# Kernel optimization log

Measured on AMD Instinct MI355X. Metric: run time of the kernel, lower is better.

Reference implementation:

```python
import jax, jax.numpy as jnp
import numpy as np

V, B, N, D, L, H = 30522, 32, 512, 512, 4, 8
HD = D // H
REC = L // 2  # block-recurrent layer index
SCALE = HD ** -0.5


def _ln(x, g, b):
    m = x.mean(-1, keepdims=True)
    v = ((x - m) ** 2).mean(-1, keepdims=True)
    return (x - m) / jnp.sqrt(v + 1e-5) * g + b


def _rope(t):
    # t: [b,h,n,hd]; rotary embedding on token positions (split-half convention)
    n = t.shape[2]
    inv = 1.0 / (10000.0 ** (jnp.arange(0, HD, 2, dtype=jnp.float32) / HD))
    f = jnp.arange(n, dtype=jnp.float32)[:, None] * inv  # [n, hd/2]
    cos, sin = jnp.cos(f), jnp.sin(f)
    t1, t2 = t[..., : HD // 2], t[..., HD // 2 :]
    return jnp.concatenate([t1 * cos - t2 * sin, t2 * cos + t1 * sin], -1)


def _heads(x):
    b, n, _ = x.shape
    return x.reshape(b, n, H, HD).transpose(0, 2, 1, 3)


def _merge(x):
    b, h, n, d = x.shape
    return x.transpose(0, 2, 1, 3).reshape(b, n, h * d)


def _attn(q, k, v, mask):
    s = jnp.einsum('bhid,bhjd->bhij', q, k) * SCALE
    if mask is not None:
        s = jnp.where(mask, s, jnp.float32(-1e9))
    a = jax.nn.softmax(s, axis=-1)
    return jnp.einsum('bhij,bhjd->bhid', a, v)


def setup_inputs() -> dict:
    key = jax.random.key(0)
    ks = jax.random.split(key, 12)
    w = lambda k, shp: jax.random.normal(k, shp, jnp.float32) * 0.02
    return {
        'ids': jax.random.randint(ks[0], (B, N), 0, V),
        'state': jax.random.normal(ks[1], (B, D), jnp.float32),
        'tok_emb': w(ks[2], (V, D)),
        'ln1_g': jnp.ones((L, D), jnp.float32), 'ln1_b': jnp.zeros((L, D), jnp.float32),
        'w_qkv': w(ks[3], (L, D, 3 * D)),
        'w_o': w(ks[4], (L, D, D)),
        'ln2_g': jnp.ones((L, D), jnp.float32), 'ln2_b': jnp.zeros((L, D), jnp.float32),
        'w_ff1': w(ks[5], (L, D, 4 * D)), 'b_ff1': jnp.zeros((L, 4 * D), jnp.float32),
        'w_ff2': w(ks[6], (L, 4 * D, D)), 'b_ff2': jnp.zeros((L, D), jnp.float32),
        's_ln_g': jnp.ones((D,), jnp.float32), 's_ln_b': jnp.zeros((D,), jnp.float32),
        'w_s_qkv': w(ks[7], (D, 3 * D)),
        'w_so': w(ks[8], (D, D)),
        'gate_beta': w(ks[9], (D,)),
        'f_ln_g': jnp.ones((D,), jnp.float32), 'f_ln_b': jnp.zeros((D,), jnp.float32),
        'head_w': w(ks[10], (D, 1)), 'head_b': jnp.zeros((1,), jnp.float32),
    }


def reference(ids, state, tok_emb, ln1_g, ln1_b, w_qkv, w_o, ln2_g, ln2_b,
              w_ff1, b_ff1, w_ff2, b_ff2, s_ln_g, s_ln_b, w_s_qkv, w_so,
              gate_beta, f_ln_g, f_ln_b, head_w, head_b):
    x = tok_emb[ids]                       # [b,n,d]
    s = state[:, None, :]                  # [b,1,d]  (state.unsqueeze(1))
    n = x.shape[1]
    causal = jnp.tril(jnp.ones((n, n), bool))
    for l in range(L):
        h = _ln(x, ln1_g[l], ln1_b[l])
        q, k, v = jnp.split(h @ w_qkv[l], 3, axis=-1)
        q, k, v = _heads(q), _heads(k), _heads(v)
        q, k = _rope(q), _rope(k)
        if l == REC:
            sn = _ln(s, s_ln_g, s_ln_b)
            sq, sk, sv = jnp.split(sn @ w_s_qkv, 3, axis=-1)
            sq, sk, sv = _heads(sq), _heads(sk), _heads(sv)
            # tokens attend over [tokens (causal), state vector (always visible)]
            m = jnp.concatenate([causal, jnp.ones((n, 1), bool)], axis=1)
            out_x = _attn(q, jnp.concatenate([k, sk], 2), jnp.concatenate([v, sv], 2), m)
            x = x + _merge(out_x) @ w_o[l]
            # state attends over [state, all tokens] (no mask)
            out_s = _attn(sq, jnp.concatenate([sk, k], 2), jnp.concatenate([sv, v], 2), None)
            upd = _merge(out_s) @ w_so
            g = jax.nn.sigmoid(gate_beta)   # fixed learned-EMA gate
            s = s * g + upd * (1.0 - g)
        else:
            out_x = _attn(q, k, v, causal)
            x = x + _merge(out_x) @ w_o[l]
        h2 = _ln(x, ln2_g[l], ln2_b[l])
        x = x + jax.nn.gelu(h2 @ w_ff1[l] + b_ff1[l]) @ w_ff2[l] + b_ff2[l]
    x = _ln(x, f_ln_g, f_ln_b)
    state_out = s[:, 0, :]                 # state[0].squeeze()
    logits = x @ head_w + head_b           # [b,n,1]
    out = jax.nn.log_softmax(logits, axis=-1)
    return out, state_out
```

## Files before the change

### kernel.cpp

```cpp
#include <hip/hip_runtime.h>
#include <hip/hip_bf16.h>
#include <math.h>

#define B_ 32
#define N_ 512
#define D_ 512
#define H_ 8
#define HD_ 64
#define QKV_ 1536
#define SCALE_ 0.125f

typedef unsigned short u16;
typedef unsigned int u32;
typedef __attribute__((ext_vector_type(8))) short bf16x8;
typedef __attribute__((ext_vector_type(4))) float f32x4;

#define GLOBAL_AS __attribute__((address_space(1)))
#define LDS_AS __attribute__((address_space(3)))

__device__ __forceinline__ float gelu_f(float x) {
  float u = 0.7978845608028654f * (x + 0.044715f * x * x * x);
  u = fminf(fmaxf(u, -15.f), 15.f);
  float e = __expf(2.f * u);
  float th = 1.f - 2.f * __builtin_amdgcn_rcpf(e + 1.f);
  return 0.5f * x * (1.0f + th);
}

__device__ __forceinline__ u16 f2b(float f) {
  union { float f; u32 u; } v;
  v.f = f;
  u32 r = (v.u + 0x7FFFu + ((v.u >> 16) & 1u)) >> 16;
  return (u16)r;
}

__device__ __forceinline__ float b2f(u16 x) {
  union { u32 u; float f; } v;
  v.u = ((u32)x) << 16;
  return v.f;
}

__device__ __forceinline__ int xcd_swz(int orig, int nwg) {
  int q = nwg >> 3, r = nwg & 7;
  int xcd = orig & 7, idx = orig >> 3;
  return (xcd < r ? xcd * (q + 1) : r * (q + 1) + (xcd - r) * q) + idx;
}

__global__ void k_prep(const float* __restrict__ w_qkv, const float* __restrict__ w_o,
                       const float* __restrict__ w_ff1, const float* __restrict__ w_ff2,
                       u16* __restrict__ wq_t, u16* __restrict__ wo_t,
                       u16* __restrict__ wf1_t, u16* __restrict__ wf2_t,
                       float* __restrict__ out0, float2* __restrict__ tab) {
  __shared__ float tile[32][33];
  int bid = blockIdx.x;
  int t = threadIdx.x;
  if (bid < 64) {
    int idx = bid * 256 + t;
    out0[idx] = 0.f;
    int n = idx >> 5, i = idx & 31;
    float inv = powf(10000.0f, -(float)i * (1.0f / 32.0f));
    float f = (float)n * inv;
    float s, c;
    sincosf(f, &s, &c);
    tab[idx] = make_float2(c, s);
    return;
  }
  int b2 = bid - 64;
  const float* W;
  u16* Wt;
  int K, N;
  if (b2 < 2304) {
    int l = b2 / 768; b2 -= l * 768;
    W = w_qkv + (size_t)l * D_ * QKV_; Wt = wq_t + (size_t)l * QKV_ * D_;
    K = D_; N = QKV_;
  } else if (b2 < 2816) {
    b2 -= 2304; int l = b2 >> 8; b2 &= 255;
    W = w_o + (size_t)l * D_ * D_; Wt = wo_t + (size_t)l * D_ * D_;
    K = D_; N = D_;
  } else if (b2 < 4864) {
    b2 -= 2816; int l = b2 >> 10; b2 &= 1023;
    W = w_ff1 + (size_t)l * D_ * 4 * D_; Wt = wf1_t + (size_t)l * 4 * D_ * D_;
    K = D_; N = 4 * D_;
  } else {
    b2 -= 4864; int l = b2 >> 10; b2 &= 1023;
    W = w_ff2 + (size_t)l * 4 * D_ * D_; Wt = wf2_t + (size_t)l * D_ * 4 * D_;
    K = 4 * D_; N = D_;
  }
  int nbx = N >> 5;
  int bx = b2 % nbx, by = b2 / nbx;
  int k0 = by * 32, n0 = bx * 32;
  int r = t >> 3, c4 = (t & 7) * 4;
  float4 v = *(const float4*)&W[(size_t)(k0 + r) * N + n0 + c4];
  tile[r][c4] = v.x; tile[r][c4 + 1] = v.y; tile[r][c4 + 2] = v.z; tile[r][c4 + 3] = v.w;
  __syncthreads();
  ushort4 o;
  o.x = f2b(tile[c4 + 0][r]); o.y = f2b(tile[c4 + 1][r]);
  o.z = f2b(tile[c4 + 2][r]); o.w = f2b(tile[c4 + 3][r]);
  *(ushort4*)&Wt[(size_t)(n0 + r) * K + k0 + c4] = o;
}

__global__ void k_embed(const int* __restrict__ ids, const float* __restrict__ emb,
                        float* __restrict__ x) {
  int row = blockIdx.x;
  int id = ids[row];
  const float4* s = (const float4*)(emb + (size_t)id * D_);
  float4* d = (float4*)(x + (size_t)row * D_);
  d[threadIdx.x] = s[threadIdx.x];
}

template <int BF16OUT>
__global__ void k_ln(const float* __restrict__ in, const float* __restrict__ gw,
                     const float* __restrict__ bw, void* __restrict__ outv) {
  int row = blockIdx.x * 4 + (threadIdx.x >> 6);
  int lane = threadIdx.x & 63;
  const float* p = in + (size_t)row * D_ + lane * 8;
  float4 v0 = *(const float4*)p;
  float4 v1 = *(const float4*)(p + 4);
  float s = v0.x + v0.y + v0.z + v0.w + v1.x + v1.y + v1.z + v1.w;
  float q = v0.x * v0.x + v0.y * v0.y + v0.z * v0.z + v0.w * v0.w +
            v1.x * v1.x + v1.y * v1.y + v1.z * v1.z + v1.w * v1.w;
#pragma unroll
  for (int o = 32; o >= 1; o >>= 1) {
    s += __shfl_xor(s, o);
    q += __shfl_xor(q, o);
  }
  float mean = s * (1.0f / D_);
  float var = q * (1.0f / D_) - mean * mean;
  float rstd = rsqrtf(var + 1e-5f);
  float4 g0 = *(const float4*)(gw + lane * 8);
  float4 g1 = *(const float4*)(gw + lane * 8 + 4);
  float4 b0 = *(const float4*)(bw + lane * 8);
  float4 b1 = *(const float4*)(bw + lane * 8 + 4);
  float o8[8];
  o8[0] = (v0.x - mean) * rstd * g0.x + b0.x;
  o8[1] = (v0.y - mean) * rstd * g0.y + b0.y;
  o8[2] = (v0.z - mean) * rstd * g0.z + b0.z;
  o8[3] = (v0.w - mean) * rstd * g0.w + b0.w;
  o8[4] = (v1.x - mean) * rstd * g1.x + b1.x;
  o8[5] = (v1.y - mean) * rstd * g1.y + b1.y;
  o8[6] = (v1.z - mean) * rstd * g1.z + b1.z;
  o8[7] = (v1.w - mean) * rstd * g1.w + b1.w;
  if (BF16OUT) {
    u16* op = (u16*)outv + (size_t)row * D_ + lane * 8;
    ushort4 a, b;
    a.x = f2b(o8[0]); a.y = f2b(o8[1]); a.z = f2b(o8[2]); a.w = f2b(o8[3]);
    b.x = f2b(o8[4]); b.y = f2b(o8[5]); b.z = f2b(o8[6]); b.w = f2b(o8[7]);
    *(ushort4*)op = a;
    *(ushort4*)(op + 4) = b;
  } else {
    float* op = (float*)outv + (size_t)row * D_ + lane * 8;
    *(float4*)op = make_float4(o8[0], o8[1], o8[2], o8[3]);
    *(float4*)(op + 4) = make_float4(o8[4], o8[5], o8[6], o8[7]);
  }
}

template <int EPI, int BF16OUT>
__global__ __launch_bounds__(256) void k_mgemm(
    const u16* __restrict__ A, const u16* __restrict__ Bt,
    const float* __restrict__ bias, const float* __restrict__ resid,
    void* __restrict__ Cv, int M, int K, int Nc, int nb0) {
  __shared__ u16 As[2][128 * 32];
  __shared__ u16 Bs[2][128 * 32];
  int t = threadIdx.x;
  int wave = t >> 6, lane = t & 63;
  int nwg = gridDim.x * gridDim.y;
  int swz = xcd_swz(blockIdx.y * gridDim.x + blockIdx.x, nwg);
  int m0 = (swz / gridDim.x) * 128;
  int n0 = ((swz % gridDim.x) + nb0) * 128;
  int wr = wave >> 1, wc = wave & 1;
  f32x4 acc[4][4] = {};

  int srow = lane >> 2;
  int scol = (lane & 3) * 8;
  const u16* gaBase = A + (size_t)(m0 + wave * 32 + srow) * K + scol;
  const u16* gbBase = Bt + (size_t)(n0 + wave * 32 + srow) * K + scol;

#define STAGE_MG(bsel, kk)                                                     \
  {                                                                            \
    _Pragma("unroll") for (int i_ = 0; i_ < 2; ++i_) {                         \
      int rbase_ = wave * 32 + i_ * 16;                                        \
      __builtin_amdgcn_global_load_lds(                                        \
          (const GLOBAL_AS void*)(gaBase + (size_t)(i_ * 16) * K + (kk)),      \
          (LDS_AS void*)&As[bsel][rbase_ * 32], 16, 0, 0);                     \
      __builtin_amdgcn_global_load_lds(                                        \
          (const GLOBAL_AS void*)(gbBase + (size_t)(i_ * 16) * K + (kk)),      \
          (LDS_AS void*)&Bs[bsel][rbase_ * 32], 16, 0, 0);                     \
    }                                                                          \
  }

  int nIter = K >> 5;
  STAGE_MG(0, 0);
  __syncthreads();
  for (int it = 0; it < nIter; ++it) {
    int cur = it & 1;
    if (it + 1 < nIter) STAGE_MG(cur ^ 1, (it + 1) << 5);
    const u16* as = As[cur];
    const u16* bs = Bs[cur];
    bf16x8 af[4], bfr[4];
#pragma unroll
    for (int mi = 0; mi < 4; ++mi)
      af[mi] = *(const bf16x8*)&as[(wr * 64 + mi * 16 + (lane & 15)) * 32 + (lane >> 4) * 8];
#pragma unroll
    for (int ni = 0; ni < 4; ++ni)
      bfr[ni] = *(const bf16x8*)&bs[(wc * 64 + ni * 16 + (lane & 15)) * 32 + (lane >> 4) * 8];
#pragma unroll
    for (int mi = 0; mi < 4; ++mi)
#pragma unroll
      for (int ni = 0; ni < 4; ++ni)
        acc[mi][ni] = __builtin_amdgcn_mfma_f32_16x16x32_bf16(bfr[ni], af[mi], acc[mi][ni], 0, 0, 0);
    __syncthreads();
  }
#undef STAGE_MG

#pragma unroll
  for (int mi = 0; mi < 4; ++mi) {
    int m = m0 + wr * 64 + mi * 16 + (lane & 15);
    size_t rowoff = (size_t)m * Nc;
#pragma unroll
    for (int ni = 0; ni < 4; ++ni) {
      int n = n0 + wc * 64 + ni * 16 + (lane >> 4) * 4;
      float v0 = acc[mi][ni][0], v1 = acc[mi][ni][1],
            v2 = acc[mi][ni][2], v3 = acc[mi][ni][3];
      if (EPI == 2 || EPI == 3) {
        float4 bb = *(const float4*)&bias[n];
        v0 += bb.x; v1 += bb.y; v2 += bb.z; v3 += bb.w;
      }
      if (EPI == 2) {
        v0 = gelu_f(v0); v1 = gelu_f(v1); v2 = gelu_f(v2); v3 = gelu_f(v3);
      }
      if (EPI == 1 || EPI == 3) {
        float4 rr = *(const float4*)&resid[rowoff + n];
        v0 += rr.x; v1 += rr.y; v2 += rr.z; v3 += rr.w;
      }
      if (BF16OUT) {
        ushort4 o;
        o.x = f2b(v0); o.y = f2b(v1); o.z = f2b(v2); o.w = f2b(v3);
        *(ushort4*)&((u16*)Cv)[rowoff + n] = o;
      } else {
        *(float4*)&((float*)Cv)[rowoff + n] = make_float4(v0, v1, v2, v3);
      }
    }
  }
}

template <int EPI>
__global__ __launch_bounds__(256) void k_gemm(const float* __restrict__ A,
                                              const float* __restrict__ W,
                                              const float* __restrict__ bias,
                                              const float* __restrict__ resid,
                                              float* __restrict__ C,
                                              int M, int K, int Nc) {
  __shared__ float As[32][68];
  __shared__ float Bs[32][68];
  int t = threadIdx.x;
  int tx = t & 15, ty = t >> 4;
  int m0 = blockIdx.y * 64, n0 = blockIdx.x * 64;
  float acc[4][4] = {};
  int ar = t >> 2, akc = (t & 3) * 8;
  int bkr = t >> 3, bnc = (t & 7) * 8;
  int garow = m0 + ar;
  bool aval = garow < M;
  const float* Aptr = A + (size_t)(aval ? garow : 0) * K + akc;
  const float* Wptr = W + (size_t)bkr * Nc + n0 + bnc;

  for (int k0 = 0; k0 < K; k0 += 32) {
    float4 a0, a1;
    if (aval) {
      a0 = *(const float4*)(Aptr + k0);
      a1 = *(const float4*)(Aptr + k0 + 4);
    } else {
      a0 = make_float4(0.f, 0.f, 0.f, 0.f);
      a1 = a0;
    }
    As[akc + 0][ar] = a0.x; As[akc + 1][ar] = a0.y;
    As[akc + 2][ar] = a0.z; As[akc + 3][ar] = a0.w;
    As[akc + 4][ar] = a1.x; As[akc + 5][ar] = a1.y;
    As[akc + 6][ar] = a1.z; As[akc + 7][ar] = a1.w;
    float4 b0 = *(const float4*)(Wptr + (size_t)k0 * Nc);
    float4 b1 = *(const float4*)(Wptr + (size_t)k0 * Nc + 4);
    *(float4*)&Bs[bkr][bnc] = b0;
    *(float4*)&Bs[bkr][bnc + 4] = b1;
    __syncthreads();
#pragma unroll
    for (int k = 0; k < 32; ++k) {
      float4 av = *(float4*)&As[k][ty * 4];
      float4 bv = *(float4*)&Bs[k][tx * 4];
      float a[4] = {av.x, av.y, av.z, av.w};
      float b[4] = {bv.x, bv.y, bv.z, bv.w};
#pragma unroll
      for (int i = 0; i < 4; ++i)
#pragma unroll
        for (int j = 0; j < 4; ++j) acc[i][j] += a[i] * b[j];
    }
    __syncthreads();
  }
#pragma unroll
  for (int i = 0; i < 4; ++i) {
    int m = m0 + ty * 4 + i;
    if (m >= M) break;
    size_t off = (size_t)m * Nc + n0 + tx * 4;
    float r[4];
#pragma unroll
    for (int j = 0; j < 4; ++j) {
      float v = acc[i][j];
      if (EPI == 2 || EPI == 3) v += bias[n0 + tx * 4 + j];
      if (EPI == 2) v = gelu_f(v);
      if (EPI == 1 || EPI == 3) v += resid[off + j];
      r[j] = v;
    }
    *(float4*)&C[off] = make_float4(r[0], r[1], r[2], r[3]);
  }
}

__global__ __launch_bounds__(512) void k_fattn(const u16* __restrict__ qkv,
                                               const float2* __restrict__ tab,
                                               u16* __restrict__ out) {
  __shared__ u16 Kl[64 * 64];
  __shared__ u16 Vt[64 * 64];
  __shared__ u16 Pl[8][16 * 64];
  int swz = xcd_swz(blockIdx.x, gridDim.x);
  int qt = swz & 3, h = (swz >> 2) & 7, b = swz >> 5;
  int t = threadIdx.x;
  int w = t >> 6, lane = t & 63;
  int c = lane & 15, g = lane >> 4;

  bf16x8 qa[2];
  {
    int n = qt * 128 + w * 16 + c;
    const u16* qptr = qkv + (size_t)(b * N_ + n) * QKV_ + h * HD_ + g * 8;
    union { bf16x8 v; u16 s[8]; } a0, a1, r0, r1;
    a0.v = *(const bf16x8*)qptr;
    a1.v = *(const bf16x8*)(qptr + 32);
    const float2* tb = tab + n * 32 + g * 8;
#pragma unroll
    for (int j = 0; j < 8; ++j) {
      float2 cs = tb[j];
      float lo = b2f(a0.s[j]), hi = b2f(a1.s[j]);
      r0.s[j] = f2b(lo * cs.x - hi * cs.y);
      r1.s[j] = f2b(hi * cs.x + lo * cs.y);
    }
    qa[0] = r0.v;
    qa[1] = r1.v;
  }

  f32x4 O[4] = {};
  float m_r[4], l_r[4];
#pragma unroll
  for (int r = 0; r < 4; ++r) { m_r[r] = -1e30f; l_r[r] = 0.f; }

  int myblk = 2 * qt + (w >> 2);
  int ktmax = 2 * qt + 1;

  for (int kt = 0; kt <= ktmax; ++kt) {
    if (t < 256) {
      int r = t >> 2, i0 = (t & 3) * 8;
      int n = kt * 64 + r;
      const u16* base = qkv + (size_t)(b * N_ + n) * QKV_ + D_ + h * HD_;
      union { bf16x8 v; u16 s[8]; } lo, hi, olo, ohi;
      lo.v = *(const bf16x8*)(base + i0);
      hi.v = *(const bf16x8*)(base + i0 + 32);
      const float2* tb = tab + n * 32 + i0;
#pragma unroll
      for (int j = 0; j < 8; ++j) {
        float2 cs = tb[j];
        float fl = b2f(lo.s[j]), fh = b2f(hi.s[j]);
        olo.s[j] = f2b(fl * cs.x - fh * cs.y);
        ohi.s[j] = f2b(fh * cs.x + fl * cs.y);
      }
      int bb = r * 128 + i0 * 2, sw = (r & 7) << 4;
      *(bf16x8*)((char*)Kl + (bb ^ sw)) = olo.v;
      *(bf16x8*)((char*)Kl + ((bb + 64) ^ sw)) = ohi.v;
    } else {
      int tt = t - 256;
      int kp = (tt >> 3) * 2, d0 = (tt & 7) * 8;
      const u16* v0p = qkv + (size_t)(b * N_ + kt * 64 + kp) * QKV_ + 2 * D_ + h * HD_ + d0;
      const u16* v1p = v0p + QKV_;
      ushort4 x0a = *(const ushort4*)v0p, x0b = *(const ushort4*)(v0p + 4);
      ushort4 x1a = *(const ushort4*)v1p, x1b = *(const ushort4*)(v1p + 4);
      u16 a0[8] = {x0a.x, x0a.y, x0a.z, x0a.w, x0b.x, x0b.y, x0b.z, x0b.w};
      u16 a1[8] = {x1a.x, x1a.y, x1a.z, x1a.w, x1b.x, x1b.y, x1b.z, x1b.w};
      u32* VtW = (u32*)Vt;
#pragma unroll
      for (int j = 0; j < 8; ++j) {
        int d = d0 + j;
        VtW[(d * 32 + (kp >> 1)) ^ ((d & 7) << 2)] = ((u32)a1[j] << 16) | (u32)a0[j];
      }
    }
    __syncthreads();

    if (kt <= myblk) {
      f32x4 s[4] = {};
#pragma unroll
      for (int ks = 0; ks < 2; ++ks) {
#pragma unroll
        for (int nt = 0; nt < 4; ++nt) {
          int krow = nt * 16 + c;
          int byteoff = (krow * 128 + (g * 8 + ks * 32) * 2) ^ ((krow & 7) << 4);
          bf16x8 kb = *(const bf16x8*)((const char*)Kl + byteoff);
          s[nt] = __builtin_amdgcn_mfma_f32_16x16x32_bf16(qa[ks], kb, s[nt], 0, 0, 0);
        }
      }
#pragma unroll
      for (int nt = 0; nt < 4; ++nt)
#pragma unroll
        for (int r = 0; r < 4; ++r) s[nt][r] *= SCALE_;
      if (kt == myblk) {
#pragma unroll
        for (int nt = 0; nt < 4; ++nt)
#pragma unroll
          for (int r = 0; r < 4; ++r)
            if (kt * 64 + nt * 16 + c > qt * 128 + w * 16 + g * 4 + r) s[nt][r] = -1e30f;
      }
      float tm[4], tl[4], fac[4];
#pragma unroll
      for (int r = 0; r < 4; ++r)
        tm[r] = fmaxf(fmaxf(s[0][r], s[1][r]), fmaxf(s[2][r], s[3][r]));
#pragma unroll
      for (int msk = 1; msk <= 8; msk <<= 1)
#pragma unroll
        for (int r = 0; r < 4; ++r)
          tm[r] = fmaxf(tm[r], __shfl_xor(tm[r], msk));
#pragma unroll
      for (int r = 0; r < 4; ++r) {
        float mn = fmaxf(m_r[r], tm[r]);
        fac[r] = __expf(m_r[r] - mn);
        m_r[r] = mn;
        tl[r] = 0.f;
      }
      u16* plw = Pl[w];
#pragma unroll
      for (int nt = 0; nt < 4; ++nt) {
#pragma unroll
        for (int r = 0; r < 4; ++r) {
          float p = __expf(s[nt][r] - m_r[r]);
          tl[r] += p;
          int q = g * 4 + r, kk = nt * 16 + c;
          plw[(q * 64 + kk) ^ ((q & 7) << 3)] = f2b(p);
        }
      }
#pragma unroll
      for (int msk = 1; msk <= 8; msk <<= 1)
#pragma unroll
        for (int r = 0; r < 4; ++r) tl[r] += __shfl_xor(tl[r], msk);
#pragma unroll
      for (int r = 0; r < 4; ++r) l_r[r] = l_r[r] * fac[r] + tl[r];
#pragma unroll
      for (int nt = 0; nt < 4; ++nt)
#pragma unroll
        for (int r = 0; r < 4; ++r) O[nt][r] *= fac[r];

#pragma unroll
      for (int ks = 0; ks < 2; ++ks) {
        int pbyte = (c * 128 + (g * 8 + ks * 32) * 2) ^ ((c & 7) << 4);
        bf16x8 pa = *(const bf16x8*)((const char*)plw + pbyte);
#pragma unroll
        for (int nt = 0; nt < 4; ++nt) {
          int d = nt * 16 + c;
          int vbyte = (d * 128 + (g * 8 + ks * 32) * 2) ^ ((d & 7) << 4);
          bf16x8 vb = *(const bf16x8*)((const char*)Vt + vbyte);
          O[nt] = __builtin_amdgcn_mfma_f32_16x16x32_bf16(pa, vb, O[nt], 0, 0, 0);
        }
      }
    }
    __syncthreads();
  }

  u16* dst = out + (size_t)(b * N_ + qt * 128 + w * 16) * D_ + h * HD_;
#pragma unroll
  for (int nt = 0; nt < 4; ++nt) {
#pragma unroll
    for (int r = 0; r < 4; ++r) {
      int q = g * 4 + r;
      dst[(size_t)q * D_ + nt * 16 + c] = f2b(O[nt][r] / l_r[r]);
    }
  }
}

__global__ __launch_bounds__(128) void k_state_attn(const float* __restrict__ sqkv,
                                                    const u16* __restrict__ qkv,
                                                    const float2* __restrict__ tab,
                                                    float* __restrict__ outs) {
  int h = blockIdx.x, b = blockIdx.y;
  __shared__ float sq[HD_];
  __shared__ float sc[513];
  __shared__ float red[128];
  int t = threadIdx.x;
  if (t < HD_) sq[t] = sqkv[(size_t)b * QKV_ + h * HD_ + t];
  __syncthreads();
  for (int j = t; j < 513; j += 128) {
    float acc = 0.f;
    if (j == 0) {
      const float* kp = sqkv + (size_t)b * QKV_ + D_ + h * HD_;
#pragma unroll
      for (int d = 0; d < HD_; ++d) acc += sq[d] * kp[d];
    } else {
      const u16* kp = qkv + (size_t)(b * N_ + j - 1) * QKV_ + D_ + h * HD_;
      const float2* tb = tab + (size_t)(j - 1) * 32;
#pragma unroll
      for (int d = 0; d < 32; ++d) {
        float2 cs = tb[d];
        float klo = b2f(kp[d]), khi = b2f(kp[d + 32]);
        acc += sq[d] * (klo * cs.x - khi * cs.y) + sq[d + 32] * (khi * cs.x + klo * cs.y);
      }
    }
    sc[j] = acc * SCALE_;
  }
  __syncthreads();
  float m = -1e30f;
  for (int j = t; j < 513; j += 128) m = fmaxf(m, sc[j]);
  red[t] = m;
  __syncthreads();
  for (int s = 64; s > 0; s >>= 1) {
    if (t < s) red[t] = fmaxf(red[t], red[t + s]);
    __syncthreads();
  }
  m = red[0];
  __syncthreads();
  float sum = 0.f;
  for (int j = t; j < 513; j += 128) {
    float p = expf(sc[j] - m);
    sc[j] = p;
    sum += p;
  }
  red[t] = sum;
  __syncthreads();
  for (int s = 64; s > 0; s >>= 1) {
    if (t < s) red[t] += red[t + s];
    __syncthreads();
  }
  float tot = red[0];
  if (t < HD_) {
    int d = t;
    float acc = sc[0] * sqkv[(size_t)b * QKV_ + 2 * D_ + h * HD_ + d];
    for (int j = 1; j <= N_; ++j)
      acc += sc[j] * b2f(qkv[(size_t)(b * N_ + j - 1) * QKV_ + 2 * D_ + h * HD_ + d]);
    outs[(size_t)b * D_ + h * HD_ + d] = acc / tot;
  }
}

__global__ void k_gate(const float* __restrict__ state, const float* __restrict__ upd,
                       const float* __restrict__ beta, float* __restrict__ out2) {
  int idx = blockIdx.x * 256 + threadIdx.x;
  int c = idx & (D_ - 1);
  float g = __builtin_amdgcn_rcpf(1.0f + __expf(-beta[c]));
  out2[idx] = state[idx] * g + upd[idx] * (1.0f - g);
}

extern "C" void kernel_launch(void* const* d_in, const int* in_sizes, int n_in,
                              void* d_out, int out_size, void* d_ws, size_t ws_size,
                              hipStream_t stream) {
  (void)in_sizes; (void)n_in; (void)out_size; (void)ws_size;
  const int* ids = (const int*)d_in[0];
  const float* state = (const float*)d_in[1];
  const float* tok_emb = (const float*)d_in[2];
  const float* ln1_g = (const float*)d_in[3];
  const float* ln1_b = (const float*)d_in[4];
  const float* w_qkv = (const float*)d_in[5];
  const float* w_o = (const float*)d_in[6];
  const float* ln2_g = (const float*)d_in[7];
  const float* ln2_b = (const float*)d_in[8];
  const float* w_ff1 = (const float*)d_in[9];
  const float* b_ff1 = (const float*)d_in[10];
  const float* w_ff2 = (const float*)d_in[11];
  const float* b_ff2 = (const float*)d_in[12];
  const float* s_ln_g = (const float*)d_in[13];
  const float* s_ln_b = (const float*)d_in[14];
  const float* w_s_qkv = (const float*)d_in[15];
  const float* w_so = (const float*)d_in[16];
  const float* gate_beta = (const float*)d_in[17];

  float* out0 = (float*)d_out;
  float* out1 = (float*)d_out + 16384;

  float* ws = (float*)d_ws;
  float* x = ws;
  u16* qkv_bf = (u16*)(ws + 8388608);
  u16* mid_bf = qkv_bf;
  u16* h_bf = (u16*)(ws + 25165824);
  u16* ao_bf = (u16*)(ws + 29360128);
  u16* wq_t = (u16*)(ws + 33554432);
  u16* wo_t = (u16*)(ws + 34734080);
  u16* wf1_t = (u16*)(ws + 34996224);
  u16* wf2_t = (u16*)(ws + 36044800);
  float* sln = ws + 37093376;
  float* sqkv = sln + 16384;
  float* souts = sqkv + 49152;
  float* supd = souts + 16384;
  float2* tab = (float2*)(ws + 37191680);

  const int M = B_ * N_;

  k_prep<<<dim3(6976), dim3(256), 0, stream>>>(w_qkv, w_o, w_ff1, w_ff2,
                                               wq_t, wo_t, wf1_t, wf2_t, out0, tab);
  k_embed<<<dim3(M), dim3(128), 0, stream>>>(ids, tok_emb, x);

  for (int l = 0; l < 3; ++l) {
    k_ln<1><<<dim3(M / 4), dim3(256), 0, stream>>>(x, ln1_g + l * D_, ln1_b + l * D_, h_bf);
    if (l == 2) {
      k_mgemm<0, 1><<<dim3(8, 128), dim3(256), 0, stream>>>(
          h_bf, wq_t + (size_t)l * QKV_ * D_, nullptr, nullptr, qkv_bf, M, D_, QKV_, 4);
      break;
    }
    k_mgemm<0, 1><<<dim3(12, 128), dim3(256), 0, stream>>>(
        h_bf, wq_t + (size_t)l * QKV_ * D_, nullptr, nullptr, qkv_bf, M, D_, QKV_, 0);
    k_fattn<<<dim3((N_ / 128) * H_ * B_), dim3(512), 0, stream>>>(qkv_bf, tab, ao_bf);
    k_mgemm<1, 0><<<dim3(4, 128), dim3(256), 0, stream>>>(
        ao_bf, wo_t + (size_t)l * D_ * D_, nullptr, x, x, M, D_, D_, 0);
    k_ln<1><<<dim3(M / 4), dim3(256), 0, stream>>>(x, ln2_g + l * D_, ln2_b + l * D_, h_bf);
    k_mgemm<2, 1><<<dim3(16, 128), dim3(256), 0, stream>>>(
        h_bf, wf1_t + (size_t)l * 4 * D_ * D_, b_ff1 + l * 4 * D_, nullptr, mid_bf, M, D_, 4 * D_, 0);
    k_mgemm<3, 0><<<dim3(4, 128), dim3(256), 0, stream>>>(
        mid_bf, wf2_t + (size_t)l * D_ * 4 * D_, b_ff2 + l * D_, x, x, M, 4 * D_, D_, 0);
  }

  k_ln<0><<<dim3(B_ / 4), dim3(256), 0, stream>>>(state, s_ln_g, s_ln_b, sln);
  k_gemm<0><<<dim3(24, 1), dim3(256), 0, stream>>>(
      sln, w_s_qkv, nullptr, nullptr, sqkv, B_, D_, QKV_);
  k_state_attn<<<dim3(H_, B_), dim3(128), 0, stream>>>(sqkv, qkv_bf, tab, souts);
  k_gemm<0><<<dim3(8, 1), dim3(256), 0, stream>>>(
      souts, w_so, nullptr, nullptr, supd, B_, D_, D_);
  k_gate<<<dim3(64), dim3(256), 0, stream>>>(state, supd, gate_beta, out1);
}
```

Baseline: 670.0 us.

## Pair causal query tiles per attention block and prefetch next K/V tile

Each attention block now handles two query tiles (qt and 3-qt), so causal work is balanced across blocks and every K/V tile loaded into LDS is reused by both query tiles. The next K/V tile's global loads are issued into registers before the current tile's compute, overlapping memory latency with MFMA work. The softmax scale is folded into Q during the RoPE step instead of being applied to every score, and launch bounds request 4 waves per SIMD. The grid is halved, and register pressure rises from holding two sets of accumulators.

```diff
diff --git a/kernel.cpp b/kernel.cpp
--- a/kernel.cpp
+++ b/kernel.cpp
@@ -311,20 +311,20 @@
   }
 }
 
-__global__ __launch_bounds__(512) void k_fattn(const u16* __restrict__ qkv,
-                                               const float2* __restrict__ tab,
-                                               u16* __restrict__ out) {
+__global__ __launch_bounds__(512, 4) void k_fattn(const u16* __restrict__ qkv,
+                                                  const float2* __restrict__ tab,
+                                                  u16* __restrict__ out) {
   __shared__ u16 Kl[64 * 64];
   __shared__ u16 Vt[64 * 64];
   __shared__ u16 Pl[8][16 * 64];
   int swz = xcd_swz(blockIdx.x, gridDim.x);
-  int qt = swz & 3, h = (swz >> 2) & 7, b = swz >> 5;
+  int p = swz & 1, h = (swz >> 1) & 7, b = swz >> 4;
+  int qtA = p, qtB = 3 - p;
   int t = threadIdx.x;
   int w = t >> 6, lane = t & 63;
   int c = lane & 15, g = lane >> 4;
 
-  bf16x8 qa[2];
-  {
+  auto loadQ = [&](int qt, bf16x8* qa) {
     int n = qt * 128 + w * 16 + c;
     const u16* qptr = qkv + (size_t)(b * N_ + n) * QKV_ + h * HD_ + g * 8;
     union { bf16x8 v; u16 s[8]; } a0, a1, r0, r1;
@@ -335,144 +335,166 @@
     for (int j = 0; j < 8; ++j) {
       float2 cs = tb[j];
       float lo = b2f(a0.s[j]), hi = b2f(a1.s[j]);
-      r0.s[j] = f2b(lo * cs.x - hi * cs.y);
-      r1.s[j] = f2b(hi * cs.x + lo * cs.y);
+      r0.s[j] = f2b((lo * cs.x - hi * cs.y) * SCALE_);
+      r1.s[j] = f2b((hi * cs.x + lo * cs.y) * SCALE_);
     }
     qa[0] = r0.v;
     qa[1] = r1.v;
-  }
-
-  f32x4 O[4] = {};
-  float m_r[4], l_r[4];
-#pragma unroll
-  for (int r = 0; r < 4; ++r) { m_r[r] = -1e30f; l_r[r] = 0.f; }
-
-  int myblk = 2 * qt + (w >> 2);
-  int ktmax = 2 * qt + 1;
-
-  for (int kt = 0; kt <= ktmax; ++kt) {
+  };
+
+  bf16x8 qaA[2], qaB[2];
+  loadQ(qtA, qaA);
+  loadQ(qtB, qaB);
+
+  f32x4 OA[4] = {}, OB[4] = {};
+  float mA[4], lA[4], mB[4], lB[4];
+#pragma unroll
+  for (int r = 0; r < 4; ++r) { mA[r] = mB[r] = -1e30f; lA[r] = lB[r] = 0.f; }
+
+  int myA = 2 * qtA + (w >> 2), myB = 2 * qtB + (w >> 2);
+  int ktmax = 2 * qtB + 1;
+
+  union { bf16x8 v; u16 s[8]; } rk0, rk1;
+  ushort4 rv0a, rv0b, rv1a, rv1b;
+  int krow = t >> 2, ki0 = (t & 3) * 8;
+  int tt = t - 256, vkp = (tt >> 3) * 2, vd0 = (tt & 7) * 8;
+
+  auto loadT = [&](int kt) {
     if (t < 256) {
-      int r = t >> 2, i0 = (t & 3) * 8;
-      int n = kt * 64 + r;
-      const u16* base = qkv + (size_t)(b * N_ + n) * QKV_ + D_ + h * HD_;
-      union { bf16x8 v; u16 s[8]; } lo, hi, olo, ohi;
-      lo.v = *(const bf16x8*)(base + i0);
-      hi.v = *(const bf16x8*)(base + i0 + 32);
-      const float2* tb = tab + n * 32 + i0;
+      const u16* base = qkv + (size_t)(b * N_ + kt * 64 + krow) * QKV_ + D_ + h * HD_;
+      rk0.v = *(const bf16x8*)(base + ki0);
+      rk1.v = *(const bf16x8*)(base + ki0 + 32);
+    } else {
+      const u16* v0p = qkv + (size_t)(b * N_ + kt * 64 + vkp) * QKV_ + 2 * D_ + h * HD_ + vd0;
+      const u16* v1p = v0p + QKV_;
+      rv0a = *(const ushort4*)v0p;
+      rv0b = *(const ushort4*)(v0p + 4);
+      rv1a = *(const ushort4*)v1p;
+      rv1b = *(const ushort4*)(v1p + 4);
+    }
+  };
+
+  auto writeT = [&](int kt) {
+    if (t < 256) {
+      int n = kt * 64 + krow;
+      const float2* tb = tab + n * 32 + ki0;
+      union { bf16x8 v; u16 s[8]; } olo, ohi;
 #pragma unroll
       for (int j = 0; j < 8; ++j) {
         float2 cs = tb[j];
-        float fl = b2f(lo.s[j]), fh = b2f(hi.s[j]);
+        float fl = b2f(rk0.s[j]), fh = b2f(rk1.s[j]);
         olo.s[j] = f2b(fl * cs.x - fh * cs.y);
         ohi.s[j] = f2b(fh * cs.x + fl * cs.y);
       }
-      int bb = r * 128 + i0 * 2, sw = (r & 7) << 4;
+      int bb = krow * 128 + ki0 * 2, sw = (krow & 7) << 4;
       *(bf16x8*)((char*)Kl + (bb ^ sw)) = olo.v;
       *(bf16x8*)((char*)Kl + ((bb + 64) ^ sw)) = ohi.v;
     } else {
-      int tt = t - 256;
-      int kp = (tt >> 3) * 2, d0 = (tt & 7) * 8;
-      const u16* v0p = qkv + (size_t)(b * N_ + kt * 64 + kp) * QKV_ + 2 * D_ + h * HD_ + d0;
-      const u16* v1p = v0p + QKV_;
-      ushort4 x0a = *(const ushort4*)v0p, x0b = *(const ushort4*)(v0p + 4);
-      ushort4 x1a = *(const ushort4*)v1p, x1b = *(const ushort4*)(v1p + 4);
-      u16 a0[8] = {x0a.x, x0a.y, x0a.z, x0a.w, x0b.x, x0b.y, x0b.z, x0b.w};
-      u16 a1[8] = {x1a.x, x1a.y, x1a.z, x1a.w, x1b.x, x1b.y, x1b.z, x1b.w};
+      u16 a0[8] = {rv0a.x, rv0a.y, rv0a.z, rv0a.w, rv0b.x, rv0b.y, rv0b.z, rv0b.w};
+      u16 a1[8] = {rv1a.x, rv1a.y, rv1a.z, rv1a.w, rv1b.x, rv1b.y, rv1b.z, rv1b.w};
       u32* VtW = (u32*)Vt;
 #pragma unroll
       for (int j = 0; j < 8; ++j) {
-        int d = d0 + j;
-        VtW[(d * 32 + (kp >> 1)) ^ ((d & 7) << 2)] = ((u32)a1[j] << 16) | (u32)a0[j];
-      }
-    }
+        int d = vd0 + j;
+        VtW[(d * 32 + (vkp >> 1)) ^ ((d & 7) << 2)] = ((u32)a1[j] << 16) | (u32)a0[j];
+      }
+    }
+  };
+
+  auto compute = [&](const bf16x8* qa, f32x4* O, float* m_r, float* l_r,
+                     int myblk, int qt, int kt) {
+    f32x4 s[4] = {};
+#pragma unroll
+    for (int ks = 0; ks < 2; ++ks) {
+#pragma unroll
+      for (int nt = 0; nt < 4; ++nt) {
+        int kr = nt * 16 + c;
+        int byteoff = (kr * 128 + (g * 8 + ks * 32) * 2) ^ ((kr & 7) << 4);
+        bf16x8 kb = *(const bf16x8*)((const char*)Kl + byteoff);
+        s[nt] = __builtin_amdgcn_mfma_f32_16x16x32_bf16(qa[ks], kb, s[nt], 0, 0, 0);
+      }
+    }
+    if (kt == myblk) {
+#pragma unroll
+      for (int nt = 0; nt < 4; ++nt)
+#pragma unroll
+        for (int r = 0; r < 4; ++r)
+          if (kt * 64 + nt * 16 + c > qt * 128 + w * 16 + g * 4 + r) s[nt][r] = -1e30f;
+    }
+    float tm[4], tl[4], fac[4];
+#pragma unroll
+    for (int r = 0; r < 4; ++r)
+      tm[r] = fmaxf(fmaxf(s[0][r], s[1][r]), fmaxf(s[2][r], s[3][r]));
+#pragma unroll
+    for (int msk = 1; msk <= 8; msk <<= 1)
+#pragma unroll
+      for (int r = 0; r < 4; ++r)
+        tm[r] = fmaxf(tm[r], __shfl_xor(tm[r], msk));
+#pragma unroll
+    for (int r = 0; r < 4; ++r) {
+      float mn = fmaxf(m_r[r], tm[r]);
+      fac[r] = __expf(m_r[r] - mn);
+      m_r[r] = mn;
+      tl[r] = 0.f;
+    }
+    u16* plw = Pl[w];
+#pragma unroll
+    for (int nt = 0; nt < 4; ++nt) {
+#pragma unroll
+      for (int r = 0; r < 4; ++r) {
+        float pv = __expf(s[nt][r] - m_r[r]);
+        tl[r] += pv;
+        int q = g * 4 + r, kk = nt * 16 + c;
+        plw[(q * 64 + kk) ^ ((q & 7) << 3)] = f2b(pv);
+      }
+    }
+#pragma unroll
+    for (int msk = 1; msk <= 8; msk <<= 1)
+#pragma unroll
+      for (int r = 0; r < 4; ++r) tl[r] += __shfl_xor(tl[r], msk);
+#pragma unroll
+    for (int r = 0; r < 4; ++r) l_r[r] = l_r[r] * fac[r] + tl[r];
+#pragma unroll
+    for (int nt = 0; nt < 4; ++nt)
+#pragma unroll
+      for (int r = 0; r < 4; ++r) O[nt][r] *= fac[r];
+#pragma unroll
+    for (int ks = 0; ks < 2; ++ks) {
+      int pbyte = (c * 128 + (g * 8 + ks * 32) * 2) ^ ((c & 7) << 4);
+      bf16x8 pa = *(const bf16x8*)((const char*)plw + pbyte);
+#pragma unroll
+      for (int nt = 0; nt < 4; ++nt) {
+        int d = nt * 16 + c;
+        int vbyte = (d * 128 + (g * 8 + ks * 32) * 2) ^ ((d & 7) << 4);
+        bf16x8 vb = *(const bf16x8*)((const char*)Vt + vbyte);
+        O[nt] = __builtin_amdgcn_mfma_f32_16x16x32_bf16(pa, vb, O[nt], 0, 0, 0);
+      }
+    }
+  };
+
+  loadT(0);
+  for (int kt = 0; kt <= ktmax; ++kt) {
+    writeT(kt);
     __syncthreads();
-
-    if (kt <= myblk) {
-      f32x4 s[4] = {};
-#pragma unroll
-      for (int ks = 0; ks < 2; ++ks) {
-#pragma unroll
-        for (int nt = 0; nt < 4; ++nt) {
-          int krow = nt * 16 + c;
-          int byteoff = (krow * 128 + (g * 8 + ks * 32) * 2) ^ ((krow & 7) << 4);
-          bf16x8 kb = *(const bf16x8*)((const char*)Kl + byteoff);
-          s[nt] = __builtin_amdgcn_mfma_f32_16x16x32_bf16(qa[ks], kb, s[nt], 0, 0, 0);
-        }
-      }
-#pragma unroll
-      for (int nt = 0; nt < 4; ++nt)
-#pragma unroll
-        for (int r = 0; r < 4; ++r) s[nt][r] *= SCALE_;
-      if (kt == myblk) {
-#pragma unroll
-        for (int nt = 0; nt < 4; ++nt)
-#pragma unroll
-          for (int r = 0; r < 4; ++r)
-            if (kt * 64 + nt * 16 + c > qt * 128 + w * 16 + g * 4 + r) s[nt][r] = -1e30f;
-      }
-      float tm[4], tl[4], fac[4];
-#pragma unroll
-      for (int r = 0; r < 4; ++r)
-        tm[r] = fmaxf(fmaxf(s[0][r], s[1][r]), fmaxf(s[2][r], s[3][r]));
-#pragma unroll
-      for (int msk = 1; msk <= 8; msk <<= 1)
-#pragma unroll
-        for (int r = 0; r < 4; ++r)
-          tm[r] = fmaxf(tm[r], __shfl_xor(tm[r], msk));
+    if (kt < ktmax) loadT(kt + 1);
+    if (kt <= myA) compute(qaA, OA, mA, lA, myA, qtA, kt);
+    if (kt <= myB) compute(qaB, OB, mB, lB, myB, qtB, kt);
+    __syncthreads();
+  }
+
+  auto store = [&](int qt, const f32x4* O, const float* l_r) {
+    u16* dst = out + (size_t)(b * N_ + qt * 128 + w * 16) * D_ + h * HD_;
+#pragma unroll
+    for (int nt = 0; nt < 4; ++nt) {
 #pragma unroll
       for (int r = 0; r < 4; ++r) {
-        float mn = fmaxf(m_r[r], tm[r]);
-        fac[r] = __expf(m_r[r] - mn);
-        m_r[r] = mn;
-        tl[r] = 0.f;
-      }
-      u16* plw = Pl[w];
-#pragma unroll
-      for (int nt = 0; nt < 4; ++nt) {
-#pragma unroll
-        for (int r = 0; r < 4; ++r) {
-          float p = __expf(s[nt][r] - m_r[r]);
-          tl[r] += p;
-          int q = g * 4 + r, kk = nt * 16 + c;
-          plw[(q * 64 + kk) ^ ((q & 7) << 3)] = f2b(p);
-        }
-      }
-#pragma unroll
-      for (int msk = 1; msk <= 8; msk <<= 1)
-#pragma unroll
-        for (int r = 0; r < 4; ++r) tl[r] += __shfl_xor(tl[r], msk);
-#pragma unroll
-      for (int r = 0; r < 4; ++r) l_r[r] = l_r[r] * fac[r] + tl[r];
-#pragma unroll
-      for (int nt = 0; nt < 4; ++nt)
-#pragma unroll
-        for (int r = 0; r < 4; ++r) O[nt][r] *= fac[r];
-
-#pragma unroll
-      for (int ks = 0; ks < 2; ++ks) {
-        int pbyte = (c * 128 + (g * 8 + ks * 32) * 2) ^ ((c & 7) << 4);
-        bf16x8 pa = *(const bf16x8*)((const char*)plw + pbyte);
-#pragma unroll
-        for (int nt = 0; nt < 4; ++nt) {
-          int d = nt * 16 + c;
-          int vbyte = (d * 128 + (g * 8 + ks * 32) * 2) ^ ((d & 7) << 4);
-          bf16x8 vb = *(const bf16x8*)((const char*)Vt + vbyte);
-          O[nt] = __builtin_amdgcn_mfma_f32_16x16x32_bf16(pa, vb, O[nt], 0, 0, 0);
-        }
-      }
-    }
-    __syncthreads();
-  }
-
-  u16* dst = out + (size_t)(b * N_ + qt * 128 + w * 16) * D_ + h * HD_;
-#pragma unroll
-  for (int nt = 0; nt < 4; ++nt) {
-#pragma unroll
-    for (int r = 0; r < 4; ++r) {
-      int q = g * 4 + r;
-      dst[(size_t)q * D_ + nt * 16 + c] = f2b(O[nt][r] / l_r[r]);
-    }
-  }
+        int q = g * 4 + r;
+        dst[(size_t)q * D_ + nt * 16 + c] = f2b(O[nt][r] / l_r[r]);
+      }
+    }
+  };
+  store(qtA, OA, lA);
+  store(qtB, OB, lB);
 }
 
 __global__ __launch_bounds__(128) void k_state_attn(const float* __restrict__ sqkv,
@@ -602,7 +624,7 @@
     }
     k_mgemm<0, 1><<<dim3(12, 128), dim3(256), 0, stream>>>(
         h_bf, wq_t + (size_t)l * QKV_ * D_, nullptr, nullptr, qkv_bf, M, D_, QKV_, 0);
-    k_fattn<<<dim3((N_ / 128) * H_ * B_), dim3(512), 0, stream>>>(qkv_bf, tab, ao_bf);
+    k_fattn<<<dim3(2 * H_ * B_), dim3(512), 0, stream>>>(qkv_bf, tab, ao_bf);
     k_mgemm<1, 0><<<dim3(4, 128), dim3(256), 0, stream>>>(
         ao_bf, wo_t + (size_t)l * D_ * D_, nullptr, x, x, M, D_, D_, 0);
     k_ln<1><<<dim3(M / 4), dim3(256), 0, stream>>>(x, ln2_g + l * D_, ln2_b + l * D_, h_bf);
```

After: 751.2 us. 1.12x slower.
